# Performance work log

Hardware: AMD Instinct MI355X
Metric: run time of the kernel (lower is better)

## Reference

```python
import jax, jax.numpy as jnp
import numpy as np

# module constants (from init_kwargs)
CS, NV, ED = 8, 4, 32          # codebook_size, num_variables, embedding_dim
VIEWS, D, KSZ = 3, 16, 3        # num_input_channels, depth, kernel_size
HW = 14                         # 7 * scale (scale=2)
CSP = 8                         # spatial of conv_shape after three valid 3x3 convs: 14->12->10->8
KSTATES = CS ** NV              # 4096 combinatorial discrete states


def _elu(x):
    return jnp.where(x > 0, x, jnp.expm1(x))


def _conv_t(x, w, b):
    # PyTorch ConvTranspose2d(stride=1, padding=0); w: (Cin, Cout, k, k)
    wf = jnp.flip(w, (2, 3)).transpose(1, 0, 2, 3)  # -> (Cout, Cin, k, k)
    p = w.shape[2] - 1
    y = jax.lax.conv_general_dilated(x, wf, (1, 1), [(p, p), (p, p)],
                                     dimension_numbers=('NCHW', 'OIHW', 'NCHW'))
    return y + b[None, :, None, None]


def setup_inputs() -> dict:
    key = jax.random.key(0)
    ks = jax.random.split(key, 10)
    rn = lambda k, shape, s=1.0: jax.random.normal(k, shape, jnp.float32) * s
    return {
        'x': rn(ks[0], (64, VIEWS, HW, HW)),
        'latent_embedding': rn(ks[1], (NV, CS, ED)),
        'lin_w': rn(ks[2], (VIEWS, ED * NV, 4 * D * CSP * CSP), 0.05),
        'lin_b': rn(ks[3], (VIEWS, 4 * D * CSP * CSP), 0.05),
        'w1': rn(ks[4], (VIEWS, 4 * D, 2 * D, KSZ, KSZ), 0.05),
        'b1': rn(ks[5], (VIEWS, 2 * D), 0.05),
        'w2': rn(ks[6], (VIEWS, 2 * D, D, KSZ, KSZ), 0.05),
        'b2': rn(ks[7], (VIEWS, D), 0.05),
        'w3': rn(ks[8], (VIEWS, D, 1, KSZ, KSZ), 0.05),
        'b3': rn(ks[9], (VIEWS, 1), 0.05),
    }


def reference(x, latent_embedding, lin_w, lin_b, w1, b1, w2, b2, w3, b3):
    # all combinations of codebook indices (itertools.product order): [K, NV]
    all_idcs = jnp.stack(
        jnp.meshgrid(*([jnp.arange(CS)] * NV), indexing='ij'), -1).reshape(-1, NV)
    # gather: z[k, v, :] = latent_embedding[v, all_idcs[k, v], :]
    z = latent_embedding[jnp.arange(NV)[None, :], all_idcs]       # [K, NV, ED]
    zf = z.reshape(KSTATES, NV * ED)                              # 'b n d -> b (n d)'

    def decode(lw, lb, W1, B1, W2, B2, W3, B3):
        h = (zf @ lw + lb).reshape(KSTATES, 4 * D, CSP, CSP)
        h = _elu(_conv_t(h, W1, B1))
        h = _elu(_conv_t(h, W2, B2))
        h = _conv_t(h, W3, B3)
        return h[:, 0]                                            # [K, HW, HW]

    m = jax.vmap(decode)(lin_w, lin_b, w1, b1, w2, b2, w3, b3)    # [views, K, HW, HW]
    m = jnp.transpose(m, (1, 0, 2, 3))                            # [K, views, HW, HW]

    # obs_logits = -0.5 * sum_{h,w} (m[None] - x[:, None])**2, computed without
    # materializing the [B, K, views, HW, HW] broadcast tensor
    m2 = jnp.sum(m * m, axis=(-2, -1))                            # [K, views]
    x2 = jnp.sum(x * x, axis=(-2, -1))                            # [B, views]
    cross = jnp.einsum('kvhw,bvhw->bkv', m, x)                    # [B, K, views]
    return -0.5 * (m2[None] + x2[:, None] - 2.0 * cross)          # [B, K, views]
```

## Files before the change

### kernel.cpp

```cpp
#include <hip/hip_runtime.h>
#include <cstddef>


typedef __attribute__((ext_vector_type(4))) float f32x4;
typedef _Float16 half8v __attribute__((ext_vector_type(8)));
typedef _Float16 half4v __attribute__((ext_vector_type(4)));
typedef _Float16 half2v __attribute__((ext_vector_type(2)));

static __device__ __forceinline__ float elu(float s) {
    float e = __expf(s) - 1.0f;
    return s > 0.f ? s : e;
}
static __device__ __forceinline__ float dot2acc(int hpair, int wpair, float acc) {
#if __has_builtin(__builtin_amdgcn_fdot2)
    return __builtin_amdgcn_fdot2(__builtin_bit_cast(half2v, hpair),
                                  __builtin_bit_cast(half2v, wpair), acc, false);
#else
    half2v h = __builtin_bit_cast(half2v, hpair);
    half2v w = __builtin_bit_cast(half2v, wpair);
    acc = fmaf((float)h.x, (float)w.x, acc);
    return fmaf((float)h.y, (float)w.y, acc);
#endif
}

__global__ __launch_bounds__(256) void pre_kernel(const float* __restrict__ x,
                                                  float* __restrict__ x2,
                                                  short* __restrict__ xB) {
    int v = blockIdx.x;
    int t = threadIdx.x;
    short* xBv = xB + v * 14336;
    for (int idx = t; idx < 14336; idx += 256) {
        int j    = idx & 7;
        int lane = (idx >> 3) & 63;
        int rest = idx >> 9;
        int s    = rest % 7;
        int nb   = rest / 7;
        int px = s * 32 + ((lane >> 4) << 3) + j;
        int b  = nb * 16 + (lane & 15);
        float val = (px < 196) ? x[(b * 3 + v) * 196 + px] : 0.f;
        _Float16 h = (_Float16)val;
        xBv[idx] = __builtin_bit_cast(short, h);
    }
    if (t < 64) {
        int b = t;
        const float* xp = x + (b * 3 + v) * 196;
        float s = 0.f;
        for (int px = 0; px < 196; ++px) s = fmaf(xp[px], xp[px], s);
        x2[v * 64 + b] = s;
    }
}

__global__ __launch_bounds__(256) void pmat_kernel(const float* __restrict__ le,
                                                   const float* __restrict__ lin_w,
                                                   float* __restrict__ P3) {
    int o  = blockIdx.x * 256 + threadIdx.x;
    int vc = blockIdx.y;
    int v  = blockIdx.z;
    int vp = vc >> 3;
    const float* lwv = lin_w + (size_t)v * 128 * 4096;
    const float* lep = le + vc * 32;
    float acc = 0.f;
#pragma unroll
    for (int e = 0; e < 32; ++e)
        acc = fmaf(lep[e], lwv[(vp * 32 + e) * 4096 + o], acc);
    P3[((size_t)v * 32 + vc) * 4096 + o] = acc;
}

__global__ __launch_bounds__(320) void fold1_kernel(const float* __restrict__ P3,
                                                    const float* __restrict__ lin_b,
                                                    const float* __restrict__ w1,
                                                    const float* __restrict__ b1,
                                                    float* __restrict__ Qcl3) {
    __shared__ float sPt[64 * 144];
    __shared__ float sW[16 * 32 * 9];
    int row = blockIdx.x;
    int v   = blockIdx.y;
    int z   = blockIdx.z;
    int t = threadIdx.x;
    const float* src = (row < 32) ? (P3 + ((size_t)v * 32 + row) * 4096)
                                  : (lin_b + v * 4096);
    float4* zp = (float4*)sPt;
    for (int i = t; i < 2304; i += 320) zp[i] = float4{0.f, 0.f, 0.f, 0.f};
    __syncthreads();
    for (int i = t; i < 4096; i += 320) {
        int ci = i >> 6, r = i & 63, y = r >> 3, xx = r & 7;
        sPt[ci * 144 + (xx + 2) * 12 + (y + 2)] = src[i];
    }
    const float* w1v = w1 + (size_t)v * 64 * 32 * 9;
    int co = t / 10, ox = t % 10;
    float acc[10];
#pragma unroll
    for (int i = 0; i < 10; ++i) acc[i] = 0.f;

    for (int c0 = z * 2; c0 < z * 2 + 2; ++c0) {
        __syncthreads();
        for (int i = t; i < 4608; i += 320) sW[i] = w1v[c0 * 4608 + i];
        __syncthreads();
#pragma unroll 2
        for (int ci = 0; ci < 16; ++ci) {
            const float* xp = sPt + (c0 * 16 + ci) * 144;
            const float* wp = sW + (ci * 32 + co) * 9;
            float wv[9];
#pragma unroll
            for (int j = 0; j < 9; ++j) wv[j] = wp[j];
#pragma unroll
            for (int b = 0; b < 3; ++b) {
                const float* colp = xp + (ox + 2 - b) * 12;
                float4 c0v = *(const float4*)(colp);
                float4 c1v = *(const float4*)(colp + 4);
                float4 c2v = *(const float4*)(colp + 8);
                float cv[12] = {c0v.x, c0v.y, c0v.z, c0v.w,
                                c1v.x, c1v.y, c1v.z, c1v.w,
                                c2v.x, c2v.y, c2v.z, c2v.w};
#pragma unroll
                for (int a = 0; a < 3; ++a) {
                    float wgt = wv[a * 3 + b];
#pragma unroll
                    for (int oy = 0; oy < 10; ++oy)
                        acc[oy] = fmaf(cv[oy + 2 - a], wgt, acc[oy]);
                }
            }
        }
    }
    float bb = (z == 0 && row == 32) ? b1[v * 32 + co] : 0.f;
    float* dst = Qcl3 + (size_t)v * 105600 + row * 3200;
#pragma unroll
    for (int oy = 0; oy < 10; ++oy)
        atomicAdd(&dst[(ox * 10 + oy) * 32 + co], acc[oy] + bb);
}

__global__ __launch_bounds__(64) void wfrag_kernel(const float* __restrict__ w2,
                                                   short* __restrict__ Wf) {
    int v = blockIdx.x;
    int lane = threadIdx.x;
    const float* w2v = w2 + v * 32 * 16 * 9;
    int co = lane & 15;
    int cibase = (lane >> 4) * 8;
#pragma unroll
    for (int tap = 0; tap < 9; ++tap)
#pragma unroll
        for (int j = 0; j < 8; ++j) {
            _Float16 h = (_Float16)w2v[((cibase + j) * 16 + co) * 9 + tap];
            Wf[(((v * 9 + tap) * 64 + lane) << 3) + j] = __builtin_bit_cast(short, h);
        }
}

__global__ __launch_bounds__(256) void fused_kernel(const float* __restrict__ Qcl3,
                                                    const short* __restrict__ Wf,
                                                    const float* __restrict__ b2,
                                                    const float* __restrict__ w3,
                                                    const float* __restrict__ b3,
                                                    short* __restrict__ Mh,
                                                    float* __restrict__ m2g) {
    __shared__ alignas(16) short sH1[196 * 40];
    __shared__ alignas(16) short sH2[16 * 392];
    __shared__ int sW3p[72];
    __shared__ float sM2;
    int k = blockIdx.x;
    int v = blockIdx.y;
    int t = threadIdx.x;
    int lane = t & 63;
    int g = lane >> 4;

    half8v bfrag[9];
#pragma unroll
    for (int tap = 0; tap < 9; ++tap)
        bfrag[tap] = *(const half8v*)(const void*)(Wf + (((v * 9 + tap) * 64 + lane) << 3));
    float bias2 = b2[v * 16 + (lane & 15)];

    if (t == 0) sM2 = 0.f;
    for (int pix = t; pix < 196; pix += 256) {
        int c = pix / 14, r = pix % 14;
        if (c < 2 || c >= 12 || r < 2 || r >= 12) {
            int4* z = (int4*)(sH1 + pix * 40);
            z[0] = int4{0,0,0,0}; z[1] = int4{0,0,0,0};
            z[2] = int4{0,0,0,0}; z[3] = int4{0,0,0,0};
        }
    }
    {
        int pix = t;
        int c = pix >> 4, r = pix & 15;
        if (c < 2 || c >= 14 || r < 2 || r >= 14) {
            int4* z = (int4*)(sH2 + c * 392 + r * 24);
            z[0] = int4{0,0,0,0}; z[1] = int4{0,0,0,0};
        }
    }
    if (t < 72) {
        int tap = t / 8, j = t % 8;
        half2v p = {(_Float16)w3[v * 144 + (2 * j) * 9 + tap],
                    (_Float16)w3[v * 144 + (2 * j + 1) * 9 + tap]};
        sW3p[t] = __builtin_bit_cast(int, p);
    }

    {
        const float* Qv = Qcl3 + (size_t)v * 105600;
        const float4* q0 = (const float4*)(Qv + ((k >> 9) & 7) * 3200);
        const float4* q1 = (const float4*)(Qv + (8  + ((k >> 6) & 7)) * 3200);
        const float4* q2 = (const float4*)(Qv + (16 + ((k >> 3) & 7)) * 3200);
        const float4* q3 = (const float4*)(Qv + (24 + (k & 7)) * 3200);
        const float4* qb = (const float4*)(Qv + 32 * 3200);
        int ci4 = (t & 7) * 4;
        int pix = t >> 3;
        int cx = pix / 10, ry = pix % 10;
        for (int i = t; i < 800; i += 256) {
            float4 a = q0[i], b = q1[i], c = q2[i], d = q3[i], e = qb[i];
            float sx = a.x + b.x + c.x + d.x + e.x;
            float sy = a.y + b.y + c.y + d.y + e.y;
            float sz = a.z + b.z + c.z + d.z + e.z;
            float sw = a.w + b.w + c.w + d.w + e.w;
            half4v o = {(_Float16)elu(sx), (_Float16)elu(sy),
                        (_Float16)elu(sz), (_Float16)elu(sw)};
            *(half4v*)(void*)(sH1 + ((cx + 2) * 14 + (ry + 2)) * 40 + ci4) = o;
            cx += 3; ry += 2;
            if (ry >= 10) { ry -= 10; ++cx; }
        }
    }
    __syncthreads();

    {
        int w = t >> 6;
        for (int tile = w; tile < 9; tile += 4) {
            int m = tile * 16 + (lane & 15);
            int cx2 = m / 12, ry2 = m % 12;
            const short* basemin = sH1 + (cx2 * 14 + ry2) * 40 + g * 8;
            f32x4 acc0 = {bias2, bias2, bias2, bias2};
            f32x4 acc1 = {0.f, 0.f, 0.f, 0.f};
#pragma unroll
            for (int a = 0; a < 3; ++a)
#pragma unroll
                for (int b = 0; b < 3; ++b) {
                    half8v af = *(const half8v*)(const void*)(basemin + ((2 - b) * 14 + (2 - a)) * 40);
                    int idx = a * 3 + b;
                    if (idx & 1)
                        acc1 = __builtin_amdgcn_mfma_f32_16x16x32_f16(af, bfrag[idx], acc1, 0, 0, 0);
                    else
                        acc0 = __builtin_amdgcn_mfma_f32_16x16x32_f16(af, bfrag[idx], acc0, 0, 0, 0);
                }
            int p0 = tile * 16 + g * 4;
            int cxp = p0 / 12, ryp = p0 % 12;
            int co = lane & 15;
#pragma unroll
            for (int r = 0; r < 4; ++r) {
                _Float16 h = (_Float16)elu(acc0[r] + acc1[r]);
                sH2[(cxp + 2) * 392 + (ryp + 2) * 24 + co] = __builtin_bit_cast(short, h);
                ++ryp; if (ryp == 12) { ryp = 0; ++cxp; }
            }
        }
    }
    __syncthreads();

    {
        float mval = 0.f;
        if (t < 196) {
            float bias3 = b3[v];
            int ry3 = t / 14, cx3 = t % 14;
            float a0 = bias3, a1 = 0.f, a2 = 0.f, a3 = 0.f;
#pragma unroll
            for (int a = 0; a < 3; ++a)
#pragma unroll
                for (int b = 0; b < 3; ++b) {
                    const short* base = sH2 + (cx3 + 2 - b) * 392 + (ry3 + 2 - a) * 24;
                    int4 lo = *(const int4*)(const void*)(base);
                    int4 hi = *(const int4*)(const void*)(base + 8);
                    const int* wp = sW3p + (a * 3 + b) * 8;
                    a0 = dot2acc(lo.x, wp[0], a0);
                    a1 = dot2acc(lo.y, wp[1], a1);
                    a2 = dot2acc(lo.z, wp[2], a2);
                    a3 = dot2acc(lo.w, wp[3], a3);
                    a0 = dot2acc(hi.x, wp[4], a0);
                    a1 = dot2acc(hi.y, wp[5], a1);
                    a2 = dot2acc(hi.z, wp[6], a2);
                    a3 = dot2acc(hi.w, wp[7], a3);
                }
            mval = (a0 + a1) + (a2 + a3);
        }
        if (t < 224) {
            _Float16 h = (_Float16)mval;
            Mh[((size_t)v * 4096 + k) * 224 + t] = __builtin_bit_cast(short, h);
        }
        float sq = mval * mval;
#pragma unroll
        for (int off = 32; off; off >>= 1) sq += __shfl_down(sq, off, 64);
        if (lane == 0) atomicAdd(&sM2, sq);
        __syncthreads();
        if (t == 0) m2g[(size_t)v * 4096 + k] = sM2;
    }
}

__global__ __launch_bounds__(256) void gemm_final_kernel(const short* __restrict__ Mh,
                                                         const short* __restrict__ xB,
                                                         const float* __restrict__ m2g,
                                                         const float* __restrict__ x2g,
                                                         float* __restrict__ out) {
    __shared__ float sC[3 * 64 * 17];
    __shared__ float sM2t[48];
    int t = threadIdx.x, lane = t & 63, nb = t >> 6;
    int k0 = blockIdx.x * 16;
    if (t < 48) {
        int v = t % 3, kk = t / 3;
        sM2t[kk * 3 + v] = m2g[(size_t)v * 4096 + k0 + kk];
    }
    int mrow = lane & 15;
    int g = lane >> 4;
#pragma unroll
    for (int v = 0; v < 3; ++v) {
        f32x4 acc = {0.f, 0.f, 0.f, 0.f};
        const short* abase = Mh + ((size_t)v * 4096 + k0 + mrow) * 224 + g * 8;
        const short* bbase = xB + (((v * 4 + nb) * 7) * 64 + lane) * 8;
#pragma unroll
        for (int s = 0; s < 7; ++s) {
            half8v af = *(const half8v*)(const void*)(abase + s * 32);
            half8v bf = *(const half8v*)(const void*)(bbase + s * 512);
            acc = __builtin_amdgcn_mfma_f32_16x16x32_f16(af, bf, acc, 0, 0, 0);
        }
        int b = nb * 16 + mrow;
#pragma unroll
        for (int r = 0; r < 4; ++r)
            sC[(v * 64 + b) * 17 + g * 4 + r] = acc[r];
    }
    __syncthreads();
    int b = t >> 2, q = t & 3;
    float x2v0 = x2g[b], x2v1 = x2g[64 + b], x2v2 = x2g[128 + b];
    float buf[12];
#pragma unroll
    for (int i = 0; i < 4; ++i) {
        int kk = q * 4 + i;
        buf[i * 3 + 0] = sC[(0 * 64 + b) * 17 + kk] - 0.5f * (sM2t[kk * 3 + 0] + x2v0);
        buf[i * 3 + 1] = sC[(1 * 64 + b) * 17 + kk] - 0.5f * (sM2t[kk * 3 + 1] + x2v1);
        buf[i * 3 + 2] = sC[(2 * 64 + b) * 17 + kk] - 0.5f * (sM2t[kk * 3 + 2] + x2v2);
    }
    float* dst = out + ((size_t)b * 4096 + k0) * 3 + q * 12;
    *(float4*)(dst)     = float4{buf[0], buf[1], buf[2],  buf[3]};
    *(float4*)(dst + 4) = float4{buf[4], buf[5], buf[6],  buf[7]};
    *(float4*)(dst + 8) = float4{buf[8], buf[9], buf[10], buf[11]};
}

extern "C" void kernel_launch(void* const* d_in, const int* in_sizes, int n_in,
                              void* d_out, int out_size, void* d_ws, size_t ws_size,
                              hipStream_t stream) {
    const float* x     = (const float*)d_in[0];
    const float* le    = (const float*)d_in[1];
    const float* lin_w = (const float*)d_in[2];
    const float* lin_b = (const float*)d_in[3];
    const float* w1    = (const float*)d_in[4];
    const float* b1    = (const float*)d_in[5];
    const float* w2    = (const float*)d_in[6];
    const float* b2    = (const float*)d_in[7];
    const float* w3    = (const float*)d_in[8];
    const float* b3    = (const float*)d_in[9];
    float* out = (float*)d_out;

    float* ws = (float*)d_ws;
    float* x2g  = ws;
    short* xB   = (short*)(ws + 192);
    float* P3   = ws + 21696;
    float* Qcl3 = ws + 414912;
    short* Mh   = (short*)(ws + 731712);
    float* m2g  = ws + 2107968;
    short* Wf   = (short*)(ws + 2120256);

    pre_kernel<<<3, 256, 0, stream>>>(x, x2g, xB);
    pmat_kernel<<<dim3(16, 32, 3), 256, 0, stream>>>(le, lin_w, P3);
    hipMemsetAsync(Qcl3, 0, 316800 * sizeof(float), stream);
    fold1_kernel<<<dim3(33, 3, 2), 320, 0, stream>>>(P3, lin_b, w1, b1, Qcl3);
    wfrag_kernel<<<3, 64, 0, stream>>>(w2, Wf);
    fused_kernel<<<dim3(4096, 3), 256, 0, stream>>>(Qcl3, Wf, b2, w3, b3, Mh, m2g);
    gemm_final_kernel<<<256, 256, 0, stream>>>(Mh, xB, m2g, x2g, out);
}
```

Before: 209.3 us.

## Precompute pairwise codebook sums so fused kernel reads two rows instead of five

Adds a pair_kernel that pre-sums the first-layer contributions of variables 0+1 and of variables 2+3 plus bias into 64-entry tables per view. The fused kernel then loads and adds only two rows per state instead of five, which cuts its global-memory traffic in the hottest kernel. fold1 now writes its two z-halves into separate buffers with plain stores, which removes the memset and the atomics. The wfrag work is merged into a wider pre_kernel grid, and the x2 reduction now uses wave shuffles. The cost is one extra small launch and larger workspace tables.

```diff
diff --git a/kernel.cpp b/kernel.cpp
--- a/kernel.cpp
+++ b/kernel.cpp
@@ -25,28 +25,45 @@
 
 __global__ __launch_bounds__(256) void pre_kernel(const float* __restrict__ x,
                                                   float* __restrict__ x2,
-                                                  short* __restrict__ xB) {
+                                                  short* __restrict__ xB,
+                                                  const float* __restrict__ w2,
+                                                  short* __restrict__ Wf) {
     int v = blockIdx.x;
+    int part = blockIdx.y;
     int t = threadIdx.x;
-    short* xBv = xB + v * 14336;
-    for (int idx = t; idx < 14336; idx += 256) {
-        int j    = idx & 7;
-        int lane = (idx >> 3) & 63;
-        int rest = idx >> 9;
-        int s    = rest % 7;
-        int nb   = rest / 7;
-        int px = s * 32 + ((lane >> 4) << 3) + j;
-        int b  = nb * 16 + (lane & 15);
-        float val = (px < 196) ? x[(b * 3 + v) * 196 + px] : 0.f;
-        _Float16 h = (_Float16)val;
-        xBv[idx] = __builtin_bit_cast(short, h);
-    }
-    if (t < 64) {
-        int b = t;
-        const float* xp = x + (b * 3 + v) * 196;
-        float s = 0.f;
-        for (int px = 0; px < 196; ++px) s = fmaf(xp[px], xp[px], s);
-        x2[v * 64 + b] = s;
+    if (part < 4) {
+        int nb = part;
+        short* xBv = xB + v * 14336 + nb * 3584;
+        for (int idx = t; idx < 3584; idx += 256) {
+            int j = idx & 7, lane = (idx >> 3) & 63, s = idx >> 9;
+            int px = s * 32 + ((lane >> 4) << 3) + j;
+            int b  = nb * 16 + (lane & 15);
+            float val = (px < 196) ? x[(b * 3 + v) * 196 + px] : 0.f;
+            _Float16 h = (_Float16)val;
+            xBv[idx] = __builtin_bit_cast(short, h);
+        }
+    } else if (part == 4) {
+        int w = t >> 6, lane = t & 63;
+        for (int b = w; b < 64; b += 4) {
+            const float* xp = x + (b * 3 + v) * 196;
+            float s = 0.f;
+            for (int px = lane; px < 196; px += 64) s = fmaf(xp[px], xp[px], s);
+#pragma unroll
+            for (int off = 32; off; off >>= 1) s += __shfl_down(s, off, 64);
+            if (lane == 0) x2[v * 64 + b] = s;
+        }
+    } else if (t < 64) {
+        int lane = t;
+        const float* w2v = w2 + v * 32 * 16 * 9;
+        int co = lane & 15;
+        int cibase = (lane >> 4) * 8;
+#pragma unroll
+        for (int tap = 0; tap < 9; ++tap)
+#pragma unroll
+            for (int j = 0; j < 8; ++j) {
+                _Float16 h = (_Float16)w2v[((cibase + j) * 16 + co) * 9 + tap];
+                Wf[(((v * 9 + tap) * 64 + lane) << 3) + j] = __builtin_bit_cast(short, h);
+            }
     }
 }
 
@@ -70,7 +87,8 @@
                                                     const float* __restrict__ lin_b,
                                                     const float* __restrict__ w1,
                                                     const float* __restrict__ b1,
-                                                    float* __restrict__ Qcl3) {
+                                                    float* __restrict__ Qa,
+                                                    float* __restrict__ Qb) {
     __shared__ float sPt[64 * 144];
     __shared__ float sW[16 * 32 * 9];
     int row = blockIdx.x;
@@ -123,29 +141,52 @@
         }
     }
     float bb = (z == 0 && row == 32) ? b1[v * 32 + co] : 0.f;
-    float* dst = Qcl3 + (size_t)v * 105600 + row * 3200;
+    float* dst = (z == 0 ? Qa : Qb) + (size_t)v * 105600 + row * 3200;
 #pragma unroll
     for (int oy = 0; oy < 10; ++oy)
-        atomicAdd(&dst[(ox * 10 + oy) * 32 + co], acc[oy] + bb);
-}
-
-__global__ __launch_bounds__(64) void wfrag_kernel(const float* __restrict__ w2,
-                                                   short* __restrict__ Wf) {
-    int v = blockIdx.x;
-    int lane = threadIdx.x;
-    const float* w2v = w2 + v * 32 * 16 * 9;
-    int co = lane & 15;
-    int cibase = (lane >> 4) * 8;
-#pragma unroll
-    for (int tap = 0; tap < 9; ++tap)
-#pragma unroll
-        for (int j = 0; j < 8; ++j) {
-            _Float16 h = (_Float16)w2v[((cibase + j) * 16 + co) * 9 + tap];
-            Wf[(((v * 9 + tap) * 64 + lane) << 3) + j] = __builtin_bit_cast(short, h);
-        }
-}
-
-__global__ __launch_bounds__(256) void fused_kernel(const float* __restrict__ Qcl3,
+        dst[(ox * 10 + oy) * 32 + co] = acc[oy] + bb;
+}
+
+__global__ __launch_bounds__(256) void pair_kernel(const float* __restrict__ Qa,
+                                                   const float* __restrict__ Qb,
+                                                   float* __restrict__ Q01,
+                                                   float* __restrict__ Q23b) {
+    int p = blockIdx.x;
+    int half = blockIdx.y;
+    int v = blockIdx.z;
+    const float4* basea = (const float4*)(Qa + (size_t)v * 105600);
+    const float4* baseb = (const float4*)(Qb + (size_t)v * 105600);
+    if (half == 0) {
+        const float4* ra = basea + (p >> 3) * 800;
+        const float4* rb = baseb + (p >> 3) * 800;
+        const float4* rc = basea + (8 + (p & 7)) * 800;
+        const float4* rd = baseb + (8 + (p & 7)) * 800;
+        float4* dst = (float4*)(Q01 + (size_t)v * 204800 + p * 3200);
+        for (int i = threadIdx.x; i < 800; i += 256) {
+            float4 a = ra[i], b = rb[i], c = rc[i], d = rd[i];
+            dst[i] = float4{a.x + b.x + c.x + d.x, a.y + b.y + c.y + d.y,
+                            a.z + b.z + c.z + d.z, a.w + b.w + c.w + d.w};
+        }
+    } else {
+        const float4* ra = basea + (16 + (p >> 3)) * 800;
+        const float4* rb = baseb + (16 + (p >> 3)) * 800;
+        const float4* rc = basea + (24 + (p & 7)) * 800;
+        const float4* rd = baseb + (24 + (p & 7)) * 800;
+        const float4* re = basea + 32 * 800;
+        const float4* rf = baseb + 32 * 800;
+        float4* dst = (float4*)(Q23b + (size_t)v * 204800 + p * 3200);
+        for (int i = threadIdx.x; i < 800; i += 256) {
+            float4 a = ra[i], b = rb[i], c = rc[i], d = rd[i], e = re[i], f = rf[i];
+            dst[i] = float4{a.x + b.x + c.x + d.x + e.x + f.x,
+                            a.y + b.y + c.y + d.y + e.y + f.y,
+                            a.z + b.z + c.z + d.z + e.z + f.z,
+                            a.w + b.w + c.w + d.w + e.w + f.w};
+        }
+    }
+}
+
+__global__ __launch_bounds__(256) void fused_kernel(const float* __restrict__ Q01,
+                                                    const float* __restrict__ Q23b,
                                                     const short* __restrict__ Wf,
                                                     const float* __restrict__ b2,
                                                     const float* __restrict__ w3,
@@ -193,23 +234,15 @@
     }
 
     {
-        const float* Qv = Qcl3 + (size_t)v * 105600;
-        const float4* q0 = (const float4*)(Qv + ((k >> 9) & 7) * 3200);
-        const float4* q1 = (const float4*)(Qv + (8  + ((k >> 6) & 7)) * 3200);
-        const float4* q2 = (const float4*)(Qv + (16 + ((k >> 3) & 7)) * 3200);
-        const float4* q3 = (const float4*)(Qv + (24 + (k & 7)) * 3200);
-        const float4* qb = (const float4*)(Qv + 32 * 3200);
+        const float4* qa = (const float4*)(Q01  + ((size_t)v * 64 + (k >> 6)) * 3200);
+        const float4* qb = (const float4*)(Q23b + ((size_t)v * 64 + (k & 63)) * 3200);
         int ci4 = (t & 7) * 4;
         int pix = t >> 3;
         int cx = pix / 10, ry = pix % 10;
         for (int i = t; i < 800; i += 256) {
-            float4 a = q0[i], b = q1[i], c = q2[i], d = q3[i], e = qb[i];
-            float sx = a.x + b.x + c.x + d.x + e.x;
-            float sy = a.y + b.y + c.y + d.y + e.y;
-            float sz = a.z + b.z + c.z + d.z + e.z;
-            float sw = a.w + b.w + c.w + d.w + e.w;
-            half4v o = {(_Float16)elu(sx), (_Float16)elu(sy),
-                        (_Float16)elu(sz), (_Float16)elu(sw)};
+            float4 a = qa[i], b = qb[i];
+            half4v o = {(_Float16)elu(a.x + b.x), (_Float16)elu(a.y + b.y),
+                        (_Float16)elu(a.z + b.z), (_Float16)elu(a.w + b.w)};
             *(half4v*)(void*)(sH1 + ((cx + 2) * 14 + (ry + 2)) * 40 + ci4) = o;
             cx += 3; ry += 2;
             if (ry >= 10) { ry -= 10; ++cx; }
@@ -353,17 +386,19 @@
     float* ws = (float*)d_ws;
     float* x2g  = ws;
     short* xB   = (short*)(ws + 192);
-    float* P3   = ws + 21696;
-    float* Qcl3 = ws + 414912;
-    short* Mh   = (short*)(ws + 731712);
-    float* m2g  = ws + 2107968;
-    short* Wf   = (short*)(ws + 2120256);
-
-    pre_kernel<<<3, 256, 0, stream>>>(x, x2g, xB);
+    short* Wf   = (short*)(ws + 21760);
+    float* P3   = ws + 28736;
+    float* Qa   = ws + 421952;
+    float* Qb   = ws + 738752;
+    float* Q01  = ws + 1055552;
+    float* Q23b = ws + 1669952;
+    short* Mh   = (short*)(ws + 2284352);
+    float* m2g  = ws + 3660608;
+
+    pre_kernel<<<dim3(3, 6), 256, 0, stream>>>(x, x2g, xB, w2, Wf);
     pmat_kernel<<<dim3(16, 32, 3), 256, 0, stream>>>(le, lin_w, P3);
-    hipMemsetAsync(Qcl3, 0, 316800 * sizeof(float), stream);
-    fold1_kernel<<<dim3(33, 3, 2), 320, 0, stream>>>(P3, lin_b, w1, b1, Qcl3);
-    wfrag_kernel<<<3, 64, 0, stream>>>(w2, Wf);
-    fused_kernel<<<dim3(4096, 3), 256, 0, stream>>>(Qcl3, Wf, b2, w3, b3, Mh, m2g);
+    fold1_kernel<<<dim3(33, 3, 2), 320, 0, stream>>>(P3, lin_b, w1, b1, Qa, Qb);
+    pair_kernel<<<dim3(64, 2, 3), 256, 0, stream>>>(Qa, Qb, Q01, Q23b);
+    fused_kernel<<<dim3(4096, 3), 256, 0, stream>>>(Q01, Q23b, Wf, b2, w3, b3, Mh, m2g);
     gemm_final_kernel<<<256, 256, 0, stream>>>(Mh, xB, m2g, x2g, out);
 }
```

Result: faster. 199.7 us (-4.5%).
